# Optimization experiments

Measured on AMD Instinct MI355X. Metric: run time of the kernel, lower is better.

Reference implementation:

```python
import jax, jax.numpy as jnp
import numpy as np

BLOCK_SIZE = 128
N_OUT = 4096
K_IN = 4096


def setup_inputs() -> dict:
    key = jax.random.key(0)
    k_x, k_w, k_s = jax.random.split(key, 3)
    x = jax.random.normal(k_x, (1, 1024, K_IN), dtype=jnp.float32)
    # ternary weights stored as int8 in {-2,-1,0,+1} (zero-point subtracted)
    weight_q = (jax.random.randint(k_w, (N_OUT, K_IN), 0, 4) - 2).astype(jnp.int8)
    n_blocks = K_IN // BLOCK_SIZE
    scales = jax.random.uniform(k_s, (N_OUT, n_blocks), dtype=jnp.float32) * 0.1 + 0.01
    return {"x": x, "weight_q": weight_q, "scales": scales}


def reference(x, weight_q, scales):
    N, K = weight_q.shape
    n_blocks = K // BLOCK_SIZE
    orig_shape = x.shape
    # [tokens, n_blocks, block_size]
    x_blocked = x.reshape(-1, n_blocks, BLOCK_SIZE).astype(jnp.float32)
    # [N, n_blocks, block_size]
    w_blocked = weight_q.reshape(N, n_blocks, BLOCK_SIZE).astype(jnp.float32)
    # per-block partial dot products: [tokens, N, n_blocks]
    raw = jnp.einsum('bki,nki->bnk', x_blocked, w_blocked)
    # apply per-(out_feature, block) scale then reduce over blocks
    out = (raw * scales).sum(axis=-1)  # [tokens, N]
    return out.astype(x.dtype).reshape(*orig_shape[:-1], N)
```

## Files before the change

kernel.cpp:

```cpp
#include <hip/hip_runtime.h>
#include <stdint.h>


#define MM 1024
#define NN 4096
#define KK 4096
#define BK 128

typedef __attribute__((ext_vector_type(4))) int intx4;
typedef __attribute__((ext_vector_type(16))) int intx16;
typedef __attribute__((ext_vector_type(4))) float floatx4;
typedef __attribute__((ext_vector_type(16))) float floatx16;

typedef const __attribute__((address_space(1))) void global_cvoid;
typedef __attribute__((address_space(3))) void lds_void;

__global__ __launch_bounds__(256) void prep(const float* __restrict__ x,
                                            const int* __restrict__ wq,
                                            char* __restrict__ xq,
                                            float* __restrict__ qrow,
                                            char* __restrict__ wb) {
    const int tid = threadIdx.x;
    if (blockIdx.x < MM) {
        const int m = blockIdx.x;
        const float* xr = x + (size_t)m * KK;
        floatx4 v[4];
        float amax = 0.f;
#pragma unroll
        for (int c = 0; c < 4; ++c) {
            v[c] = *(const floatx4*)(xr + (c * 256 + tid) * 4);
#pragma unroll
            for (int e = 0; e < 4; ++e) amax = fmaxf(amax, fabsf(v[c][e]));
        }
#pragma unroll
        for (int off = 32; off; off >>= 1) amax = fmaxf(amax, __shfl_down(amax, off));
        __shared__ float wmax[4];
        if ((tid & 63) == 0) wmax[tid >> 6] = amax;
        __syncthreads();
        amax = fmaxf(fmaxf(wmax[0], wmax[1]), fmaxf(wmax[2], wmax[3]));
        amax = fmaxf(amax, 1e-20f);
        const float qinv = 127.0f / amax;
        if (tid == 0) qrow[m] = amax / 127.0f;
#pragma unroll
        for (int c = 0; c < 4; ++c) {
            int p = 0;
#pragma unroll
            for (int e = 0; e < 4; ++e) {
                float r = rintf(v[c][e] * qinv);
                r = fminf(fmaxf(r, -127.f), 127.f);
                p |= ((int)r & 255) << (8 * e);
            }
            *(int*)(xq + (size_t)m * KK + (c * 256 + tid) * 4) = p;
        }
    } else {
        const int blk = blockIdx.x - MM;
#pragma unroll
        for (int c = 0; c < 4; ++c) {
            size_t c4 = (size_t)blk * 1024 + c * 256 + tid;
            intx4 a = ((const intx4*)wq)[c4];
            ((int*)wb)[c4] = (a[0] & 255) | ((a[1] & 255) << 8) |
                             ((a[2] & 255) << 16) | (a[3] << 24);
        }
    }
}

__global__ __launch_bounds__(256, 2) void q8_gemm(const char* __restrict__ xq,
                                                  const char* __restrict__ wb,
                                                  const float* __restrict__ qrow,
                                                  const float* __restrict__ scales,
                                                  float* __restrict__ out) {
    __shared__ char As[2][64 * BK];
    __shared__ float Sl[128 * 33];

    const int tid  = threadIdx.x;
    const int lane = tid & 63;
    const int wave = tid >> 6;
    const int l31  = lane & 31;
    const int hi   = lane >> 5;
    const int sw   = lane & 7;
    const int wn   = wave * 32;

    const int bid = blockIdx.x;
    const int xcd = bid & 7, loc = bid >> 3;
    const int nT = xcd * 4 + (loc & 3);
    const int mT = loc >> 2;
    const int mBase = mT * 64, nBase = nT * 128;

    const int rg = lane >> 3;
    const int cs = (lane & 7) ^ rg;
    const char* gA = xq + (size_t)(mBase + wave * 16 + rg) * KK + cs * 16;
    const int ldsRowA = wave * 16;

    const char* gBrow = wb + (size_t)(nBase + wn + l31) * KK + hi * 16;

    floatx16 fac0, fac1;
#pragma unroll
    for (int r = 0; r < 16; ++r) { fac0[r] = 0.f; fac1[r] = 0.f; }

#define STAGE_A(BUF, SLAB)                                                      \
    {                                                                           \
        _Pragma("unroll")                                                       \
        for (int t = 0; t < 2; ++t)                                             \
            __builtin_amdgcn_global_load_lds(                                   \
                (global_cvoid*)(gA + (size_t)(t * 8) * KK + (SLAB) * BK),       \
                (lds_void*)&As[BUF][(ldsRowA + t * 8) * BK], 16, 0, 0);         \
    }

#define LOAD_B(BV, SLAB)                                                        \
    {                                                                           \
        _Pragma("unroll")                                                       \
        for (int kp = 0; kp < 4; ++kp)                                          \
            BV[kp] = *(const intx4*)(gBrow + (size_t)(SLAB) * BK + kp * 32);    \
    }

#define COMPUTE(BUF, SLAB, BV)                                                  \
    {                                                                           \
        const float sf = Sl[(wn + l31) * 33 + (SLAB)];                          \
        intx16 iacc0, iacc1;                                                    \
        __builtin_amdgcn_s_setprio(1);                                          \
        _Pragma("unroll")                                                       \
        for (int kp = 0; kp < 4; ++kp) {                                        \
            const int kc = (((kp * 2) + hi) ^ sw) << 4;                         \
            intx4 av0 = *(const intx4*)&As[BUF][l31 * BK + kc];                 \
            intx4 av1 = *(const intx4*)&As[BUF][(32 + l31) * BK + kc];          \
            const int kq = ((kp * 2) + hi) >> 1;    \
            (void)kq;                                                           \
            if (kp == 0) {                                                      \
                intx16 z = {0, 0, 0, 0, 0, 0, 0, 0, 0, 0, 0, 0, 0, 0, 0, 0};    \
                iacc0 = __builtin_amdgcn_mfma_i32_32x32x32_i8(av0, BV[kp], z, 0, 0, 0); \
                iacc1 = __builtin_amdgcn_mfma_i32_32x32x32_i8(av1, BV[kp], z, 0, 0, 0); \
            } else {                                                            \
                iacc0 = __builtin_amdgcn_mfma_i32_32x32x32_i8(av0, BV[kp], iacc0, 0, 0, 0); \
                iacc1 = __builtin_amdgcn_mfma_i32_32x32x32_i8(av1, BV[kp], iacc1, 0, 0, 0); \
            }                                                                   \
        }                                                                       \
        __builtin_amdgcn_s_setprio(0);                                          \
        _Pragma("unroll")                                                       \
        for (int r = 0; r < 16; ++r) {                                          \
            fac0[r] += (float)iacc0[r] * sf;                                    \
            fac1[r] += (float)iacc1[r] * sf;                                    \
        }                                                                       \
    }


    intx4 bvA[4], bvB[4];
    STAGE_A(0, 0)
    LOAD_B(bvA, 0)
    for (int t = tid; t < 4096; t += 256) {
        int nl = t >> 5, b = t & 31;
        Sl[nl * 33 + b] = scales[(size_t)(nBase + nl) * 32 + b];
    }
    __syncthreads();

    const int NIT = KK / BK;
    for (int it = 0; it < NIT; it += 2) {
        if (it + 1 < NIT) { STAGE_A(1, it + 1) LOAD_B(bvB, it + 1) }
        COMPUTE(0, it, bvA)
        __syncthreads();
        if (it + 2 < NIT) { STAGE_A(0, it + 2) LOAD_B(bvA, it + 2) }
        COMPUTE(1, it + 1, bvB)
        __syncthreads();
    }

#pragma unroll
    for (int g = 0; g < 4; ++g) {
        floatx4 qv0 = *(const floatx4*)(qrow + mBase + g * 8 + hi * 4);
        floatx4 qv1 = *(const floatx4*)(qrow + mBase + 32 + g * 8 + hi * 4);
#pragma unroll
        for (int r = 0; r < 4; ++r) {
            const int m0 = mBase + g * 8 + hi * 4 + r;
            out[(size_t)m0 * NN + nBase + wn + l31]        = fac0[g * 4 + r] * qv0[r];
            out[(size_t)(m0 + 32) * NN + nBase + wn + l31] = fac1[g * 4 + r] * qv1[r];
        }
    }
#undef STAGE_A
#undef LOAD_B
#undef COMPUTE
}

extern "C" void kernel_launch(void* const* d_in, const int* in_sizes, int n_in,
                              void* d_out, int out_size, void* d_ws, size_t ws_size,
                              hipStream_t stream) {
    const float* x      = (const float*)d_in[0];
    const int*   wq     = (const int*)d_in[1];
    const float* scales = (const float*)d_in[2];
    float*       out    = (float*)d_out;

    char*  xq   = (char*)d_ws;
    float* qrow = (float*)((char*)d_ws + (size_t)MM * KK);
    char*  wb   = (char*)d_ws + (size_t)MM * KK + 4096;

    prep<<<MM + (size_t)NN * KK / 16 / 256, 256, 0, stream>>>(x, wq, xq, qrow, wb);
    q8_gemm<<<(MM / 64) * (NN / 128), 256, 0, stream>>>(xq, wb, qrow, scales, out);
}
```

Measured before the change: 151.9 us.

## Deepen B register prefetch to four slabs with manual waitcnt pipeline

Restructures the GEMM main loop into a 4-phase software pipeline. B fragments are prefetched three slabs ahead in registers. Per-row scales are loaded directly from global into registers instead of staging them through LDS. __syncthreads is replaced by explicit s_waitcnt vmcnt counts plus s_barrier, so more global loads stay in flight, and the LDS scale table and its initial load are removed. In exchange it uses more VGPRs for the extra B buffers, which may affect occupancy at 2 waves/SIMD. The hand-counted vmcnt values must match the issued loads exactly, and the wrapped slab indices do redundant loads past the end.

Measured after the change: 168.2 us. +10.7%, slower.

```diff
diff --git a/kernel.cpp b/kernel.cpp
--- a/kernel.cpp
+++ b/kernel.cpp
@@ -13,6 +13,8 @@
 typedef __attribute__((ext_vector_type(16))) float floatx16;
 
 typedef const __attribute__((address_space(1))) void global_cvoid;
+typedef const __attribute__((address_space(1))) intx4 g_intx4;
+typedef const __attribute__((address_space(1))) floatx4 g_floatx4;
 typedef __attribute__((address_space(3))) void lds_void;
 
 __global__ __launch_bounds__(256) void prep(const float* __restrict__ x,
@@ -70,7 +72,6 @@
                                                   const float* __restrict__ scales,
                                                   float* __restrict__ out) {
     __shared__ char As[2][64 * BK];
-    __shared__ float Sl[128 * 33];
 
     const int tid  = threadIdx.x;
     const int lane = tid & 63;
@@ -89,9 +90,10 @@
     const int rg = lane >> 3;
     const int cs = (lane & 7) ^ rg;
     const char* gA = xq + (size_t)(mBase + wave * 16 + rg) * KK + cs * 16;
-    const int ldsRowA = wave * 16;
+    const int ldsRow = wave * 16;
 
     const char* gBrow = wb + (size_t)(nBase + wn + l31) * KK + hi * 16;
+    const float* scrow = scales + (size_t)(nBase + wn + l31) * 32;
 
     floatx16 fac0, fac1;
 #pragma unroll
@@ -102,20 +104,19 @@
         _Pragma("unroll")                                                       \
         for (int t = 0; t < 2; ++t)                                             \
             __builtin_amdgcn_global_load_lds(                                   \
-                (global_cvoid*)(gA + (size_t)(t * 8) * KK + (SLAB) * BK),       \
-                (lds_void*)&As[BUF][(ldsRowA + t * 8) * BK], 16, 0, 0);         \
+                (global_cvoid*)(gA + (size_t)(t * 8) * KK + (size_t)(SLAB) * BK),\
+                (lds_void*)&As[BUF][(ldsRow + t * 8) * BK], 16, 0, 0);          \
     }
 
 #define LOAD_B(BV, SLAB)                                                        \
     {                                                                           \
         _Pragma("unroll")                                                       \
-        for (int kp = 0; kp < 4; ++kp)                                          \
-            BV[kp] = *(const intx4*)(gBrow + (size_t)(SLAB) * BK + kp * 32);    \
-    }
-
-#define COMPUTE(BUF, SLAB, BV)                                                  \
-    {                                                                           \
-        const float sf = Sl[(wn + l31) * 33 + (SLAB)];                          \
+        for (int q = 0; q < 4; ++q)                                             \
+            BV[q] = *(g_intx4*)(gBrow + (size_t)(SLAB) * BK + q * 32);          \
+    }
+
+#define COMPUTE(BUF, BV, SF)                                                    \
+    {                                                                           \
         intx16 iacc0, iacc1;                                                    \
         __builtin_amdgcn_s_setprio(1);                                          \
         _Pragma("unroll")                                                       \
@@ -123,12 +124,10 @@
             const int kc = (((kp * 2) + hi) ^ sw) << 4;                         \
             intx4 av0 = *(const intx4*)&As[BUF][l31 * BK + kc];                 \
             intx4 av1 = *(const intx4*)&As[BUF][(32 + l31) * BK + kc];          \
-            const int kq = ((kp * 2) + hi) >> 1;    \
-            (void)kq;                                                           \
             if (kp == 0) {                                                      \
                 intx16 z = {0, 0, 0, 0, 0, 0, 0, 0, 0, 0, 0, 0, 0, 0, 0, 0};    \
-                iacc0 = __builtin_amdgcn_mfma_i32_32x32x32_i8(av0, BV[kp], z, 0, 0, 0); \
-                iacc1 = __builtin_amdgcn_mfma_i32_32x32x32_i8(av1, BV[kp], z, 0, 0, 0); \
+                iacc0 = __builtin_amdgcn_mfma_i32_32x32x32_i8(av0, BV[0], z, 0, 0, 0); \
+                iacc1 = __builtin_amdgcn_mfma_i32_32x32x32_i8(av1, BV[0], z, 0, 0, 0); \
             } else {                                                            \
                 iacc0 = __builtin_amdgcn_mfma_i32_32x32x32_i8(av0, BV[kp], iacc0, 0, 0, 0); \
                 iacc1 = __builtin_amdgcn_mfma_i32_32x32x32_i8(av1, BV[kp], iacc1, 0, 0, 0); \
@@ -137,29 +136,44 @@
         __builtin_amdgcn_s_setprio(0);                                          \
         _Pragma("unroll")                                                       \
         for (int r = 0; r < 16; ++r) {                                          \
-            fac0[r] += (float)iacc0[r] * sf;                                    \
-            fac1[r] += (float)iacc1[r] * sf;                                    \
+            fac0[r] += (float)iacc0[r] * (SF);                                  \
+            fac1[r] += (float)iacc1[r] * (SF);                                  \
         }                                                                       \
     }
 
-
-    intx4 bvA[4], bvB[4];
+#define PHASE(PH, BASE, BV, SF, WAITN)                                          \
+    {                                                                           \
+        STAGE_A((PH + 1) & 1, ((BASE) + (PH) + 1) & 31)                         \
+        __builtin_amdgcn_sched_barrier(0);                                      \
+        COMPUTE((PH) & 1, BV, SF)                                               \
+        LOAD_B(BV, ((BASE) + (PH) + 4) & 31)                                    \
+        asm volatile("s_waitcnt vmcnt(" #WAITN ")" ::: "memory");               \
+        __builtin_amdgcn_s_barrier();                                           \
+    }
+
+    intx4 bv0[4], bv1[4], bv2[4], bv3[4];
     STAGE_A(0, 0)
-    LOAD_B(bvA, 0)
-    for (int t = tid; t < 4096; t += 256) {
-        int nl = t >> 5, b = t & 31;
-        Sl[nl * 33 + b] = scales[(size_t)(nBase + nl) * 32 + b];
-    }
-    __syncthreads();
-
-    const int NIT = KK / BK;
-    for (int it = 0; it < NIT; it += 2) {
-        if (it + 1 < NIT) { STAGE_A(1, it + 1) LOAD_B(bvB, it + 1) }
-        COMPUTE(0, it, bvA)
-        __syncthreads();
-        if (it + 2 < NIT) { STAGE_A(0, it + 2) LOAD_B(bvA, it + 2) }
-        COMPUTE(1, it + 1, bvB)
-        __syncthreads();
+    __builtin_amdgcn_sched_barrier(0);
+    LOAD_B(bv0, 0) LOAD_B(bv1, 1) LOAD_B(bv2, 2) LOAD_B(bv3, 3)
+    floatx4 scv_c = *(g_floatx4*)(scrow + 0);
+    floatx4 scv_n = *(g_floatx4*)(scrow + 4);
+    asm volatile("s_waitcnt vmcnt(18)" ::: "memory");
+    __builtin_amdgcn_s_barrier();
+
+    for (int base = 0; base < 32; base += 4) {
+        PHASE(0, base, bv0, scv_c[0], 4)
+        PHASE(1, base, bv1, scv_c[1], 4)
+        PHASE(2, base, bv2, scv_c[2], 4)
+        {
+            STAGE_A(0, (base + 4) & 31)
+            __builtin_amdgcn_sched_barrier(0);
+            COMPUTE(1, bv3, scv_c[3])
+            LOAD_B(bv3, (base + 7) & 31)
+            scv_c = scv_n;
+            scv_n = *(g_floatx4*)(scrow + (((base >> 2) + 2) & 7) * 4);
+            asm volatile("s_waitcnt vmcnt(5)" ::: "memory");
+            __builtin_amdgcn_s_barrier();
+        }
     }
 
 #pragma unroll
@@ -176,6 +190,7 @@
 #undef STAGE_A
 #undef LOAD_B
 #undef COMPUTE
+#undef PHASE
 }
 
 extern "C" void kernel_launch(void* const* d_in, const int* in_sizes, int n_in,
```
